# Optimization experiments

Measured on AMD Instinct MI355X. Metric: run time of the kernel, lower is better.

## Reference

```python
import jax, jax.numpy as jnp
import numpy as np

B, IN_DIM, N_NODES, N_LEAVES, N_ACTIONS = 131072, 128, 511, 512, 16


def setup_inputs() -> dict:
    key = jax.random.key(0)
    k1, k2, k3, k4 = jax.random.split(key, 4)
    x = jax.random.normal(k1, (B, IN_DIM), dtype=jnp.float32)
    W1 = jax.random.normal(k2, (N_NODES, IN_DIM), dtype=jnp.float32) * 0.1
    b1 = jax.random.normal(k3, (N_NODES,), dtype=jnp.float32) * 0.1
    W2 = jax.random.normal(k4, (N_LEAVES, 2 * N_NODES), dtype=jnp.float32) * 0.05
    # leaf -> action assignment; arange % n_actions guarantees every group non-empty
    leaf_actions = (jnp.arange(N_LEAVES) % N_ACTIONS).astype(jnp.int32)
    return {"x": x, "W1": W1, "b1": b1, "W2": W2, "leaf_actions": leaf_actions}


def reference(x, W1, b1, W2, leaf_actions):
    # linear1
    h = x @ W1.T + b1                      # [B, N_NODES]
    # relu(h) || relu(-h)
    z = jnp.concatenate([jax.nn.relu(h), jax.nn.relu(-h)], axis=1)  # [B, 2*N_NODES]
    # linear2 (no bias)
    y = z @ W2.T                           # [B, N_LEAVES]
    # grouped segment-max over leaf columns, grouped by action id
    pooled = jax.ops.segment_max(y.T, leaf_actions, num_segments=N_ACTIONS).T  # [B, N_ACTIONS]
    return jax.nn.softmax(pooled, axis=-1)
```

## Files before the change

kernel.cpp:

```cpp
#include <hip/hip_runtime.h>
#include <hip/hip_bf16.h>

typedef unsigned short u16;
typedef unsigned int u32;
typedef __attribute__((ext_vector_type(8))) short bf16x8;
typedef __attribute__((ext_vector_type(16))) float f32x16;

#define NROWS   131072
#define KDIM    128
#define NNODES  511
#define NACT    16

__device__ __forceinline__ u16 f2b(float v) {
  return __builtin_bit_cast(u16, __float2bfloat16(v));
}

union Frag {
  bf16x8 v;
  u16    u[8];
  int4   i;
  int    d[4];
};

#define Z16 {0.f,0.f,0.f,0.f,0.f,0.f,0.f,0.f,0.f,0.f,0.f,0.f,0.f,0.f,0.f,0.f}

__global__ void prep_k(const float* __restrict__ W1, const float* __restrict__ W2,
                       const float* __restrict__ b1, u16* __restrict__ w1f,
                       u16* __restrict__ wgt, float* __restrict__ b1r) {
  int bid = blockIdx.x, t = threadIdx.x;
  if (bid < 256) {
    int o = bid * 256 + t;
    int j = o & 7, l = (o >> 3) & 63, ks = (o >> 9) & 7, nt = o >> 12;
    int node = nt * 32 + (l & 31);
    int k = ks * 16 + ((l >> 5) << 3) + j;
    w1f[o] = f2b(node < NNODES ? W1[node * KDIM + k] : 0.f);
  } else if (bid < 2304) {
    int o = (bid - 256) * 256 + t;
    int j = o & 7, l = (o >> 3) & 63, lt = (o >> 9) & 15, s = o >> 13;
    int type = s & 1, kstep = s >> 1;
    int leaf = lt * 32 + (l & 31);
    int n = kstep * 16 + ((l >> 5) << 3) + j;
    float va = 0.f, vb = 0.f;
    if (n < NNODES) {
      va = W2[leaf * (2 * NNODES) + n];
      vb = W2[leaf * (2 * NNODES) + NNODES + n];
    }
    wgt[o] = f2b(type ? 0.5f * (va + vb) : 0.5f * (va - vb));
  } else {
    int o = (bid - 2304) * 256 + t;
    int r = o & 15, hi2 = (o >> 4) & 1, nt = o >> 5;
    int node = nt * 32 + (r & 3) + 8 * (r >> 2) + 4 * hi2;
    b1r[o] = (node < NNODES) ? b1[node] : 0.f;
  }
}

__global__ __launch_bounds__(512, 2) void fused_k(const float* __restrict__ x,
                                                  const u16* __restrict__ w1f,
                                                  const u16* __restrict__ wgt,
                                                  const float* __restrict__ b1r,
                                                  float* __restrict__ out) {
  __shared__ u16 Hh[4 * 32 * 64 * 8];
  __shared__ u16 Ss[2 * 16 * 64 * 8];

  const int t = threadIdx.x, w = t >> 6, l = t & 63;
  const int la = l & 31, hi = l >> 5;
  const int rg = blockIdx.x;

  {
    const float* xb = x + (size_t)rg * 128 * KDIM;
#pragma unroll
    for (int i = 0; i < 4; ++i) {
      int f = w * 4 + i;
      int rt = f >> 3, ks = f & 7;
      const float* src = xb + (rt * 32 + la) * KDIM + ks * 16 + hi * 8;
      float4 v0 = *(const float4*)src;
      float4 v1 = *(const float4*)(src + 4);
      Frag fr;
      fr.u[0] = f2b(v0.x); fr.u[1] = f2b(v0.y); fr.u[2] = f2b(v0.z); fr.u[3] = f2b(v0.w);
      fr.u[4] = f2b(v1.x); fr.u[5] = f2b(v1.y); fr.u[6] = f2b(v1.z); fr.u[7] = f2b(v1.w);
      *(int4*)&Ss[f * 512 + l * 8] = fr.i;
    }
  }
  __syncthreads();

  {
    const int nt0 = w * 2;
    Frag a1[16];
#pragma unroll
    for (int q = 0; q < 16; ++q)
      a1[q].i = *(const int4*)(w1f + ((size_t)((nt0 + (q >> 3)) * 8 + (q & 7)) * 64 + l) * 8);
    float4 bias[2][4];
#pragma unroll
    for (int n2 = 0; n2 < 2; ++n2)
#pragma unroll
      for (int g = 0; g < 4; ++g)
        bias[n2][g] = *(const float4*)(b1r + ((nt0 + n2) * 2 + hi) * 16 + g * 4);

#pragma unroll 1
    for (int rt = 0; rt < 4; ++rt) {
      f32x16 c0 = Z16, c1 = Z16;
#pragma unroll
      for (int ks = 0; ks < 8; ++ks) {
        Frag b;
        b.i = *(const int4*)&Ss[(rt * 8 + ks) * 512 + l * 8];
        c0 = __builtin_amdgcn_mfma_f32_32x32x16_bf16(a1[ks].v, b.v, c0, 0, 0, 0);
        c1 = __builtin_amdgcn_mfma_f32_32x32x16_bf16(a1[8 + ks].v, b.v, c1, 0, 0, 0);
      }
#pragma unroll
      for (int n2 = 0; n2 < 2; ++n2) {
        int nt = nt0 + n2;
#pragma unroll
        for (int p = 0; p < 8; ++p) {
          int q = p >> 1, e = p & 1;
          int r0 = 4 * q + 2 * e;
          float bv0 = e ? bias[n2][q].z : bias[n2][q].x;
          float bv1 = e ? bias[n2][q].w : bias[n2][q].y;
          float v0 = (n2 ? c1[r0]     : c0[r0])     + bv0;
          float v1 = (n2 ? c1[r0 + 1] : c0[r0 + 1]) + bv1;
          int n32 = 8 * q + 4 * hi + 2 * e;
          int c_h = n32 >> 4, jj = n32 & 15;
          u32 pkv = (u32)f2b(v0) | ((u32)f2b(v1) << 16);
          *(u32*)&Hh[((rt * 32 + nt * 2 + c_h) * 64 + ((jj >> 3) << 5) + la) * 8 + (jj & 6)] = pkv;
        }
      }
    }
  }
  __syncthreads();

#pragma unroll
  for (int i = 0; i < 2; ++i) {
    int f = w * 2 + i;
    __builtin_amdgcn_global_load_lds(
        (const __attribute__((address_space(1))) void*)(wgt + (size_t)f * 512 + l * 8),
        (__attribute__((address_space(3))) void*)&Ss[f * 512], 16, 0, 0);
  }
  __syncthreads();

  f32x16 acc[4][2] = {{Z16, Z16}, {Z16, Z16}, {Z16, Z16}, {Z16, Z16}};
  Frag ha[4];

#pragma unroll 1
  for (int s = 0; s < 64; ++s) {
    if (s < 63) {
#pragma unroll
      for (int i = 0; i < 2; ++i) {
        int f = w * 2 + i;
        __builtin_amdgcn_global_load_lds(
            (const __attribute__((address_space(1))) void*)(wgt + (size_t)((s + 1) * 16 + f) * 512 + l * 8),
            (__attribute__((address_space(3))) void*)&Ss[((s + 1) & 1) * 8192 + f * 512], 16, 0, 0);
      }
    }
    if (!(s & 1)) {
      int kstep = s >> 1;
#pragma unroll
      for (int rt = 0; rt < 4; ++rt)
        ha[rt].i = *(const int4*)&Hh[((rt * 32 + kstep) * 64 + l) * 8];
    } else {
#pragma unroll
      for (int rt = 0; rt < 4; ++rt)
#pragma unroll
        for (int d = 0; d < 4; ++d) ha[rt].d[d] &= 0x7FFF7FFF;
    }
    Frag wb0, wb1;
    wb0.i = *(const int4*)&Ss[(s & 1) * 8192 + (w * 2 + 0) * 512 + l * 8];
    wb1.i = *(const int4*)&Ss[(s & 1) * 8192 + (w * 2 + 1) * 512 + l * 8];
#pragma unroll
    for (int rt = 0; rt < 4; ++rt) {
      acc[rt][0] = __builtin_amdgcn_mfma_f32_32x32x16_bf16(ha[rt].v, wb0.v, acc[rt][0], 0, 0, 0);
      acc[rt][1] = __builtin_amdgcn_mfma_f32_32x32x16_bf16(ha[rt].v, wb1.v, acc[rt][1], 0, 0, 0);
    }
    __syncthreads();
  }

  float* Hred = (float*)Hh;
#pragma unroll
  for (int rt = 0; rt < 4; ++rt)
#pragma unroll
    for (int r = 0; r < 16; ++r) {
      int row = rt * 32 + (r & 3) + 8 * (r >> 2) + 4 * hi;
      float v = fmaxf(acc[rt][0][r], acc[rt][1][r]);
      Hred[(w * 128 + row) * 32 + (la ^ ((r & 3) << 2))] = v;
    }
  __syncthreads();
  {
    int row = t >> 2, ag = t & 3;
    int xr = (row & 3) << 2;
    float p0 = -1e30f, p1 = -1e30f, p2 = -1e30f, p3 = -1e30f;
#pragma unroll
    for (int ww = 0; ww < 8; ++ww)
#pragma unroll
      for (int h2 = 0; h2 < 2; ++h2) {
        float4 v = *(const float4*)&Hred[(ww * 128 + row) * 32 + ((h2 * 16 + ag * 4) ^ xr)];
        p0 = fmaxf(p0, v.x); p1 = fmaxf(p1, v.y);
        p2 = fmaxf(p2, v.z); p3 = fmaxf(p3, v.w);
      }
    float m = fmaxf(fmaxf(p0, p1), fmaxf(p2, p3));
    m = fmaxf(m, __shfl_xor(m, 1));
    m = fmaxf(m, __shfl_xor(m, 2));
    float e0 = __expf(p0 - m), e1 = __expf(p1 - m), e2 = __expf(p2 - m), e3 = __expf(p3 - m);
    float ssum = e0 + e1 + e2 + e3;
    ssum += __shfl_xor(ssum, 1);
    ssum += __shfl_xor(ssum, 2);
    float inv = 1.f / ssum;
    float4 o4;
    o4.x = e0 * inv; o4.y = e1 * inv; o4.z = e2 * inv; o4.w = e3 * inv;
    *(float4*)(out + ((size_t)rg * 128 + row) * NACT + ag * 4) = o4;
  }
}

extern "C" void kernel_launch(void* const* d_in, const int* in_sizes, int n_in,
                              void* d_out, int out_size, void* d_ws, size_t ws_size,
                              hipStream_t stream) {
  const float* x  = (const float*)d_in[0];
  const float* W1 = (const float*)d_in[1];
  const float* b1 = (const float*)d_in[2];
  const float* W2 = (const float*)d_in[3];

  char* ws = (char*)d_ws;
  u16*   w1f = (u16*)ws;
  u16*   wgt = (u16*)(ws + 131072);
  float* b1r = (float*)(ws + 131072 + 1048576);

  prep_k <<<dim3(2308), dim3(256), 0, stream>>>(W1, W2, b1, w1f, wgt, b1r);
  fused_k<<<dim3(NROWS / 128), dim3(512), 0, stream>>>(x, w1f, wgt, b1r, (float*)d_out);
}
```

Baseline: 267.9 us.

## Load W2 fragments directly into registers with prefetch instead of LDS staging

```diff
diff --git a/kernel.cpp b/kernel.cpp
--- a/kernel.cpp
+++ b/kernel.cpp
@@ -60,7 +60,7 @@
                                                   const float* __restrict__ b1r,
                                                   float* __restrict__ out) {
   __shared__ u16 Hh[4 * 32 * 64 * 8];
-  __shared__ u16 Ss[2 * 16 * 64 * 8];
+  __shared__ u16 Ss[32 * 64 * 8];
 
   const int t = threadIdx.x, w = t >> 6, l = t & 63;
   const int la = l & 31, hi = l >> 5;
@@ -127,50 +127,44 @@
   }
   __syncthreads();
 
-#pragma unroll
-  for (int i = 0; i < 2; ++i) {
-    int f = w * 2 + i;
-    __builtin_amdgcn_global_load_lds(
-        (const __attribute__((address_space(1))) void*)(wgt + (size_t)f * 512 + l * 8),
-        (__attribute__((address_space(3))) void*)&Ss[f * 512], 16, 0, 0);
-  }
-  __syncthreads();
-
   f32x16 acc[4][2] = {{Z16, Z16}, {Z16, Z16}, {Z16, Z16}, {Z16, Z16}};
-  Frag ha[4];
+
+#define WADDR(k, type, i) (wgt + ((size_t)((k) * 32 + (type) * 16 + w * 2 + (i))) * 512 + l * 8)
+
+  Frag Ad0, Ad1, As0, As1, Bd0, Bd1, Bs0, Bs1;
+  Ad0.i = *(const int4*)WADDR(0, 0, 0); Ad1.i = *(const int4*)WADDR(0, 0, 1);
+  As0.i = *(const int4*)WADDR(0, 1, 0); As1.i = *(const int4*)WADDR(0, 1, 1);
+  Bd0.i = *(const int4*)WADDR(1, 0, 0); Bd1.i = *(const int4*)WADDR(1, 0, 1);
+  Bs0.i = *(const int4*)WADDR(1, 1, 0); Bs1.i = *(const int4*)WADDR(1, 1, 1);
+
+#define KSTEP(kk, D0, D1, S0, S1, kpf)                                                            \
+  {                                                                                               \
+    Frag ha[4];                                                                                   \
+    _Pragma("unroll") for (int rt = 0; rt < 4; ++rt)                                              \
+      ha[rt].i = *(const int4*)&Hh[((rt * 32 + (kk)) * 64 + l) * 8];                              \
+    _Pragma("unroll") for (int rt = 0; rt < 4; ++rt) {                                            \
+      acc[rt][0] = __builtin_amdgcn_mfma_f32_32x32x16_bf16(ha[rt].v, D0.v, acc[rt][0], 0, 0, 0);  \
+      acc[rt][1] = __builtin_amdgcn_mfma_f32_32x32x16_bf16(ha[rt].v, D1.v, acc[rt][1], 0, 0, 0);  \
+    }                                                                                             \
+    _Pragma("unroll") for (int rt = 0; rt < 4; ++rt)                                              \
+      _Pragma("unroll") for (int d = 0; d < 4; ++d) ha[rt].d[d] &= 0x7FFF7FFF;                    \
+    _Pragma("unroll") for (int rt = 0; rt < 4; ++rt) {                                            \
+      acc[rt][0] = __builtin_amdgcn_mfma_f32_32x32x16_bf16(ha[rt].v, S0.v, acc[rt][0], 0, 0, 0);  \
+      acc[rt][1] = __builtin_amdgcn_mfma_f32_32x32x16_bf16(ha[rt].v, S1.v, acc[rt][1], 0, 0, 0);  \
+    }                                                                                             \
+    if ((kpf) < 32) {                                                                             \
+      D0.i = *(const int4*)WADDR((kpf), 0, 0); D1.i = *(const int4*)WADDR((kpf), 0, 1);           \
+      S0.i = *(const int4*)WADDR((kpf), 1, 0); S1.i = *(const int4*)WADDR((kpf), 1, 1);           \
+    }                                                                                             \
+  }
 
 #pragma unroll 1
-  for (int s = 0; s < 64; ++s) {
-    if (s < 63) {
-#pragma unroll
-      for (int i = 0; i < 2; ++i) {
-        int f = w * 2 + i;
-        __builtin_amdgcn_global_load_lds(
-            (const __attribute__((address_space(1))) void*)(wgt + (size_t)((s + 1) * 16 + f) * 512 + l * 8),
-            (__attribute__((address_space(3))) void*)&Ss[((s + 1) & 1) * 8192 + f * 512], 16, 0, 0);
-      }
-    }
-    if (!(s & 1)) {
-      int kstep = s >> 1;
-#pragma unroll
-      for (int rt = 0; rt < 4; ++rt)
-        ha[rt].i = *(const int4*)&Hh[((rt * 32 + kstep) * 64 + l) * 8];
-    } else {
-#pragma unroll
-      for (int rt = 0; rt < 4; ++rt)
-#pragma unroll
-        for (int d = 0; d < 4; ++d) ha[rt].d[d] &= 0x7FFF7FFF;
-    }
-    Frag wb0, wb1;
-    wb0.i = *(const int4*)&Ss[(s & 1) * 8192 + (w * 2 + 0) * 512 + l * 8];
-    wb1.i = *(const int4*)&Ss[(s & 1) * 8192 + (w * 2 + 1) * 512 + l * 8];
-#pragma unroll
-    for (int rt = 0; rt < 4; ++rt) {
-      acc[rt][0] = __builtin_amdgcn_mfma_f32_32x32x16_bf16(ha[rt].v, wb0.v, acc[rt][0], 0, 0, 0);
-      acc[rt][1] = __builtin_amdgcn_mfma_f32_32x32x16_bf16(ha[rt].v, wb1.v, acc[rt][1], 0, 0, 0);
-    }
-    __syncthreads();
-  }
+  for (int k = 0; k < 32; k += 2) {
+    KSTEP(k,     Ad0, Ad1, As0, As1, k + 2);
+    KSTEP(k + 1, Bd0, Bd1, Bs0, Bs1, k + 3);
+  }
+
+  __syncthreads();
 
   float* Hred = (float*)Hh;
 #pragma unroll
```

New measurement: 223.0 us. -16.8%, faster.
